# Performance work log

Measured on AMD Instinct MI355X. Metric: run time of the kernel, lower is better.

The kernel has to match this reference:

```python
import jax, jax.numpy as jnp
import numpy as np

N = 4_000_000   # number of rows
F = 32          # num_feature
P = 100_000     # number of segments (p)


def setup_inputs() -> dict:
    key = jax.random.key(0)
    k1, k2, k3, k4 = jax.random.split(key, 4)
    feats = jax.random.normal(k1, (N, F), dtype=jnp.float32)
    # nn.Linear(num_feature, 1): weight [1, F], bias [1]
    W = jax.random.normal(k2, (1, F), dtype=jnp.float32) / np.sqrt(F)
    b = jax.random.normal(k3, (1,), dtype=jnp.float32) * 0.01
    idx = jax.random.randint(k4, (N,), 0, P, dtype=jnp.int64)
    return {"feats": feats, "W": W, "b": b, "idx": idx, "p": P}


def reference(feats, W, b, idx, p):
    # per-row linear projection to a scalar: r[n] = feats[n] . W[0] + b[0]
    r = jnp.einsum("nf,f->n", feats, W[0]) + b[0]
    # c starts at zeros and is updated when r >= c[t]  =>  c = max(0, segment_max(r))
    seg = jax.ops.segment_max(r, idx, num_segments=p)  # empty segments -> -inf
    return jnp.maximum(seg, 0.0)
```

## Files before the change

kernel.cpp:

```cpp
#include <hip/hip_runtime.h>


typedef float f32x4 __attribute__((ext_vector_type(4)));

__global__ __launch_bounds__(256, 8) void miniNN_seglinmax_kernel(
    const f32x4* __restrict__ feats4,
    const float* __restrict__ W,
    const float* __restrict__ b,
    const int*   __restrict__ idx,
    int*         __restrict__ out_i,
    int          n_rows)
{
    const int lane = threadIdx.x & 63;
    const int sub  = lane & 7;
    const int j    = lane >> 3;
    const int gwid = blockIdx.x * (blockDim.x >> 6) + (threadIdx.x >> 6);
    const int nw   = gridDim.x * (blockDim.x >> 6);

    const f32x4 wv  = ((const f32x4*)W)[sub];
    const float bias = b[0];

    const int nsuper = n_rows >> 5;
    for (int sg = gwid; sg < nsuper; sg += nw) {
        const f32x4* p = feats4 + (sg << 8) + lane;
        const f32x4 v0 = __builtin_nontemporal_load(p);
        const f32x4 v1 = __builtin_nontemporal_load(p + 64);
        const f32x4 v2 = __builtin_nontemporal_load(p + 128);
        const f32x4 v3 = __builtin_nontemporal_load(p + 192);

        float s0 = v0.x * wv.x + v0.y * wv.y + v0.z * wv.z + v0.w * wv.w;
        float s1 = v1.x * wv.x + v1.y * wv.y + v1.z * wv.z + v1.w * wv.w;
        float s2 = v2.x * wv.x + v2.y * wv.y + v2.z * wv.z + v2.w * wv.w;
        float s3 = v3.x * wv.x + v3.y * wv.y + v3.z * wv.z + v3.w * wv.w;

        s0 += __shfl_xor(s0, 1); s0 += __shfl_xor(s0, 2); s0 += __shfl_xor(s0, 4);
        s1 += __shfl_xor(s1, 1); s1 += __shfl_xor(s1, 2); s1 += __shfl_xor(s1, 4);
        s2 += __shfl_xor(s2, 1); s2 += __shfl_xor(s2, 2); s2 += __shfl_xor(s2, 4);
        s3 += __shfl_xor(s3, 1); s3 += __shfl_xor(s3, 2); s3 += __shfl_xor(s3, 4);

        if (sub == 0) {
            const int rowbase = (sg << 5) + j;
            const int i0 = __builtin_nontemporal_load(idx + rowbase);
            const int i1 = __builtin_nontemporal_load(idx + rowbase + 8);
            const int i2 = __builtin_nontemporal_load(idx + rowbase + 16);
            const int i3 = __builtin_nontemporal_load(idx + rowbase + 24);
            const float r0 = s0 + bias;
            const float r1 = s1 + bias;
            const float r2 = s2 + bias;
            const float r3 = s3 + bias;
            if (r0 > 0.0f) atomicMax(out_i + i0, __float_as_int(r0));
            if (r1 > 0.0f) atomicMax(out_i + i1, __float_as_int(r1));
            if (r2 > 0.0f) atomicMax(out_i + i2, __float_as_int(r2));
            if (r3 > 0.0f) atomicMax(out_i + i3, __float_as_int(r3));
        }
    }

    const int tail_start = nsuper << 5;
    const int gtid = blockIdx.x * blockDim.x + threadIdx.x;
    const int row  = tail_start + gtid;
    if (row < n_rows) {
        const float* f = (const float*)feats4 + (long long)row * 32;
        float r = bias;
        #pragma unroll
        for (int k = 0; k < 32; ++k) r += f[k] * W[k];
        if (r > 0.0f) atomicMax(out_i + idx[row], __float_as_int(r));
    }
}

extern "C" void kernel_launch(void* const* d_in, const int* in_sizes, int n_in,
                              void* d_out, int out_size, void* d_ws, size_t ws_size,
                              hipStream_t stream) {
    const float* feats = (const float*)d_in[0];
    const float* W     = (const float*)d_in[1];
    const float* b     = (const float*)d_in[2];
    const int*   idx   = (const int*)d_in[3];
    const int n_rows   = in_sizes[0] / 32;

    (void)hipMemsetAsync(d_out, 0, (size_t)out_size * sizeof(float), stream);

    const int nsuper = n_rows >> 5;
    int best_blocks = 2048;
    long long best_cost = 0x7fffffffffffffffLL;
    for (int blk = 256; blk <= 2048; ++blk) {
        const long long waves = (long long)blk * 4;
        const long long iters = (nsuper + waves - 1) / waves;
        const long long cost  = waves * iters;
        if (cost < best_cost || (cost == best_cost && blk > best_blocks)) {
            best_cost = cost; best_blocks = blk;
        }
    }

    miniNN_seglinmax_kernel<<<best_blocks, 256, 0, stream>>>(
        (const f32x4*)feats, W, b, idx, (int*)d_out, n_rows);
}
```

Baseline: 114.5 us.

## Process 64 rows per wave iteration and spread atomics across all lanes

Each wave now loads 8 float4 vectors per iteration, covering 64 rows instead of 32, which doubles the loads in flight per thread. After the shuffle reduction, a select tree gives each lane one distinct row's dot product. All 64 lanes then load their own index and issue the atomicMax, so only one eighth of lanes no longer does the index loads and atomics. Launch bounds drop to 4 blocks per SM to allow more registers, at the cost of lower occupancy.

New measurement: 115.5 us. About the same (+0.9%).

```diff
diff --git a/kernel.cpp b/kernel.cpp
--- a/kernel.cpp
+++ b/kernel.cpp
@@ -3,7 +3,7 @@
 
 typedef float f32x4 __attribute__((ext_vector_type(4)));
 
-__global__ __launch_bounds__(256, 8) void miniNN_seglinmax_kernel(
+__global__ __launch_bounds__(256, 4) void miniNN_seglinmax_kernel(
     const f32x4* __restrict__ feats4,
     const float* __restrict__ W,
     const float* __restrict__ b,
@@ -11,51 +11,61 @@
     int*         __restrict__ out_i,
     int          n_rows)
 {
-    const int lane = threadIdx.x & 63;
-    const int sub  = lane & 7;
-    const int j    = lane >> 3;
+    const int l    = threadIdx.x & 63;
     const int gwid = blockIdx.x * (blockDim.x >> 6) + (threadIdx.x >> 6);
     const int nw   = gridDim.x * (blockDim.x >> 6);
 
-    const f32x4 wv  = ((const f32x4*)W)[sub];
+    const f32x4 wv  = ((const f32x4*)W)[l & 7];
     const float bias = b[0];
 
-    const int nsuper = n_rows >> 5;
+    const int myrow = (l >> 3) + ((l & 7) << 3);
+
+    const int nsuper = n_rows >> 6;
     for (int sg = gwid; sg < nsuper; sg += nw) {
-        const f32x4* p = feats4 + (sg << 8) + lane;
+        const f32x4* p = feats4 + (sg << 9) + l;
         const f32x4 v0 = __builtin_nontemporal_load(p);
         const f32x4 v1 = __builtin_nontemporal_load(p + 64);
         const f32x4 v2 = __builtin_nontemporal_load(p + 128);
         const f32x4 v3 = __builtin_nontemporal_load(p + 192);
+        const f32x4 v4 = __builtin_nontemporal_load(p + 256);
+        const f32x4 v5 = __builtin_nontemporal_load(p + 320);
+        const f32x4 v6 = __builtin_nontemporal_load(p + 384);
+        const f32x4 v7 = __builtin_nontemporal_load(p + 448);
 
-        float s0 = v0.x * wv.x + v0.y * wv.y + v0.z * wv.z + v0.w * wv.w;
-        float s1 = v1.x * wv.x + v1.y * wv.y + v1.z * wv.z + v1.w * wv.w;
-        float s2 = v2.x * wv.x + v2.y * wv.y + v2.z * wv.z + v2.w * wv.w;
-        float s3 = v3.x * wv.x + v3.y * wv.y + v3.z * wv.z + v3.w * wv.w;
+        float s[8];
+        s[0] = v0.x * wv.x + v0.y * wv.y + v0.z * wv.z + v0.w * wv.w;
+        s[1] = v1.x * wv.x + v1.y * wv.y + v1.z * wv.z + v1.w * wv.w;
+        s[2] = v2.x * wv.x + v2.y * wv.y + v2.z * wv.z + v2.w * wv.w;
+        s[3] = v3.x * wv.x + v3.y * wv.y + v3.z * wv.z + v3.w * wv.w;
+        s[4] = v4.x * wv.x + v4.y * wv.y + v4.z * wv.z + v4.w * wv.w;
+        s[5] = v5.x * wv.x + v5.y * wv.y + v5.z * wv.z + v5.w * wv.w;
+        s[6] = v6.x * wv.x + v6.y * wv.y + v6.z * wv.z + v6.w * wv.w;
+        s[7] = v7.x * wv.x + v7.y * wv.y + v7.z * wv.z + v7.w * wv.w;
 
-        s0 += __shfl_xor(s0, 1); s0 += __shfl_xor(s0, 2); s0 += __shfl_xor(s0, 4);
-        s1 += __shfl_xor(s1, 1); s1 += __shfl_xor(s1, 2); s1 += __shfl_xor(s1, 4);
-        s2 += __shfl_xor(s2, 1); s2 += __shfl_xor(s2, 2); s2 += __shfl_xor(s2, 4);
-        s3 += __shfl_xor(s3, 1); s3 += __shfl_xor(s3, 2); s3 += __shfl_xor(s3, 4);
+        #pragma unroll
+        for (int k = 0; k < 8; ++k) {
+            s[k] += __shfl_xor(s[k], 1);
+            s[k] += __shfl_xor(s[k], 2);
+            s[k] += __shfl_xor(s[k], 4);
+        }
 
-        if (sub == 0) {
-            const int rowbase = (sg << 5) + j;
-            const int i0 = __builtin_nontemporal_load(idx + rowbase);
-            const int i1 = __builtin_nontemporal_load(idx + rowbase + 8);
-            const int i2 = __builtin_nontemporal_load(idx + rowbase + 16);
-            const int i3 = __builtin_nontemporal_load(idx + rowbase + 24);
-            const float r0 = s0 + bias;
-            const float r1 = s1 + bias;
-            const float r2 = s2 + bias;
-            const float r3 = s3 + bias;
-            if (r0 > 0.0f) atomicMax(out_i + i0, __float_as_int(r0));
-            if (r1 > 0.0f) atomicMax(out_i + i1, __float_as_int(r1));
-            if (r2 > 0.0f) atomicMax(out_i + i2, __float_as_int(r2));
-            if (r3 > 0.0f) atomicMax(out_i + i3, __float_as_int(r3));
-        }
+        const bool b0 = (l & 1) != 0;
+        const bool b1 = (l & 2) != 0;
+        const bool b2 = (l & 4) != 0;
+        const float t0 = b0 ? s[1] : s[0];
+        const float t1 = b0 ? s[3] : s[2];
+        const float t2 = b0 ? s[5] : s[4];
+        const float t3 = b0 ? s[7] : s[6];
+        const float u0 = b1 ? t1 : t0;
+        const float u1 = b1 ? t3 : t2;
+        const float dot = b2 ? u1 : u0;
+
+        const int i  = __builtin_nontemporal_load(idx + (sg << 6) + myrow);
+        const float r = dot + bias;
+        if (r > 0.0f) atomicMax(out_i + i, __float_as_int(r));
     }
 
-    const int tail_start = nsuper << 5;
+    const int tail_start = nsuper << 6;
     const int gtid = blockIdx.x * blockDim.x + threadIdx.x;
     const int row  = tail_start + gtid;
     if (row < n_rows) {
@@ -78,7 +88,7 @@
 
     (void)hipMemsetAsync(d_out, 0, (size_t)out_size * sizeof(float), stream);
 
-    const int nsuper = n_rows >> 5;
+    const int nsuper = n_rows >> 6;
     int best_blocks = 2048;
     long long best_cost = 0x7fffffffffffffffLL;
     for (int blk = 256; blk <= 2048; ++blk) {
```
